# Performance work log

Measured on AMD Instinct MI355X. Metric: run time of the kernel, lower is better.

## Reference

```python
import jax, jax.numpy as jnp
import numpy as np

VOCAB = 32000
EMB = 32
HID = 16
SEQ = 128
BATCH = 32


def setup_inputs() -> dict:
    key = jax.random.key(0)
    k1, k2, k3, k4, k5 = jax.random.split(key, 5)
    return {
        "input_batch": jax.random.randint(k1, (SEQ, BATCH), 0, VOCAB, dtype=jnp.int32),
        "lookup": jax.random.normal(k2, (VOCAB, EMB), dtype=jnp.float32) * 0.1,
        "weight_x": jax.random.normal(k3, (EMB, HID), dtype=jnp.float32) * 0.1,
        "weight_h": jax.random.normal(k4, (HID, HID), dtype=jnp.float32) * 0.1,
        "weight_o": jax.random.normal(k5, (HID, VOCAB), dtype=jnp.float32) * 0.1,
    }


def reference(input_batch, lookup, weight_x, weight_h, weight_o):
    # X: [S, B, EMB]; torch code uses .data -> embedding lookup is detached
    X = jax.lax.stop_gradient(lookup[input_batch])
    batch = input_batch.shape[1]
    H0 = jnp.ones((batch, HID), dtype=jnp.float32)  # torch inits H to ones

    def step(H, x_t):
        H_new = jnp.tanh(x_t @ weight_x + H @ weight_h)  # [B, HID]
        logits = H_new @ weight_o                         # [B, V]
        return H_new, jax.nn.log_softmax(logits, axis=-1)  # log(softmax(x))

    _, out = jax.lax.scan(step, H0, X)  # out: [S, B, V]
    return out
```

## Files before the change

### kernel.cpp

```cpp
#include <hip/hip_runtime.h>

#define VOCAB 32000
#define EMB 32
#define HID 16
#define SEQ 128
#define BATCH 32
#define NROW (SEQ * BATCH)

typedef float f32x2 __attribute__((ext_vector_type(2)));
typedef float f32x4 __attribute__((ext_vector_type(4)));

__global__ __launch_bounds__(512) void embed_xw(
    const int* __restrict__ idx, const float* __restrict__ lookup,
    const float* __restrict__ Wx, float* __restrict__ A)
{
    __shared__ float sWx[EMB][HID];
    const int tid = threadIdx.x;
    ((float*)sWx)[tid] = Wx[tid];
    __syncthreads();

    const int g = blockIdx.x * 512 + tid;
    const int row = g >> 4, j = g & 15;
    const float* xr = lookup + (size_t)idx[row] * EMB;
    float a0 = 0.f, a1 = 0.f;
    #pragma unroll
    for (int e = 0; e < EMB; e += 2) {
        a0 += xr[e] * sWx[e][j];
        a1 += xr[e + 1] * sWx[e + 1][j];
    }
    A[g] = a0 + a1;
}

__global__ __launch_bounds__(512) void rnn_recur(
    const float* __restrict__ A, const float* __restrict__ Wh,
    float* __restrict__ Hout)
{
    __shared__ __align__(16) float sH[BATCH][HID];

    const int tid = threadIdx.x;
    const int b = tid >> 4, j = tid & 15;

    float wh[HID];
    #pragma unroll
    for (int k = 0; k < HID; ++k) wh[k] = Wh[k * HID + j];

    sH[b][j] = 1.0f;
    __syncthreads();

    float a0r = A[0 * 512 + tid];
    float a1r = A[1 * 512 + tid];
    float a2r = A[2 * 512 + tid];
    float a3r = A[3 * 512 + tid];

#define RNN_STEP(AR, T)                                                     \
    {                                                                       \
        float acc = AR;                                                     \
        if ((T) + 4 < SEQ) AR = A[((T) + 4) * 512 + tid];                   \
        const f32x4* sH4 = (const f32x4*)&sH[b][0];                         \
        f32x4 h0 = sH4[0], h1 = sH4[1], h2v = sH4[2], h3v = sH4[3];         \
        acc += h0.x * wh[0] + h0.y * wh[1] + h0.z * wh[2] + h0.w * wh[3];   \
        acc += h1.x * wh[4] + h1.y * wh[5] + h1.z * wh[6] + h1.w * wh[7];   \
        acc += h2v.x * wh[8] + h2v.y * wh[9] + h2v.z * wh[10]               \
             + h2v.w * wh[11];                                              \
        acc += h3v.x * wh[12] + h3v.y * wh[13] + h3v.z * wh[14]             \
             + h3v.w * wh[15];                                              \
        float e2 = __expf(2.f * acc);          \
        float h = 1.f - 2.f / (e2 + 1.f);                                   \
        sH[b][j] = h;                                                       \
        Hout[(T) * 512 + tid] = h;                                          \
    }

    for (int t = 0; t < SEQ; t += 4) {
        RNN_STEP(a0r, t + 0)
        RNN_STEP(a1r, t + 1)
        RNN_STEP(a2r, t + 2)
        RNN_STEP(a3r, t + 3)
    }
#undef RNN_STEP
}

#define CSL 500

__global__ __launch_bounds__(512, 4) void sum_exp_partial(
    const float* __restrict__ H, const float* __restrict__ Wo,
    float* __restrict__ P)
{
    __shared__ float part[8][64];

    const int tid = threadIdx.x;
    const int lane = tid & 63;
    const int wave = tid >> 6;
    const int rgrp = blockIdx.x >> 3;
    const int cchunk = blockIdx.x & 7;
    const int row0 = rgrp * 64;
    const int c0 = __builtin_amdgcn_readfirstlane(cchunk * 4000 + wave * CSL);

    f32x2 hp[HID];
    {
        const f32x4* h4 = (const f32x4*)(H + (size_t)(row0 + lane) * HID);
        #pragma unroll
        for (int q = 0; q < 4; ++q) {
            f32x4 hv = h4[q];
            hp[4 * q + 0] = f32x2{hv.x, hv.x};
            hp[4 * q + 1] = f32x2{hv.y, hv.y};
            hp[4 * q + 2] = f32x2{hv.z, hv.z};
            hp[4 * q + 3] = f32x2{hv.w, hv.w};
        }
    }

    const float* wbase = Wo + c0;
    float acc0 = 0.f, acc1 = 0.f, acc2 = 0.f, acc3 = 0.f;
    for (int v = 0; v < CSL; v += 4) {
        f32x2 a01 = {0.f, 0.f}, a23 = {0.f, 0.f};
        #pragma unroll
        for (int k = 0; k < HID; ++k) {
            f32x4 w4 = *(const f32x4*)(wbase + (size_t)k * VOCAB + v);
            asm("v_pk_fma_f32 %0, %1, %2, %0"
                : "+v"(a01) : "v"(hp[k]), "s"(w4.xy));
            asm("v_pk_fma_f32 %0, %1, %2, %0"
                : "+v"(a23) : "v"(hp[k]), "s"(w4.zw));
        }
        acc0 += __expf(a01.x); acc1 += __expf(a01.y);
        acc2 += __expf(a23.x); acc3 += __expf(a23.y);
    }

    part[wave][lane] = (acc0 + acc1) + (acc2 + acc3);
    __syncthreads();
    if (wave == 0) {
        float tot = 0.f;
        #pragma unroll
        for (int w = 0; w < 8; ++w) tot += part[w][lane];
        P[(size_t)cchunk * NROW + row0 + lane] = tot;
    }
}

#define RV 64
#define VSK 2048

__global__ __launch_bounds__(512, 4) void write_logits(
    const float* __restrict__ H, const float* __restrict__ Wo,
    const float* __restrict__ P, float* __restrict__ out)
{
    __shared__ __align__(16) float sH[RV * HID];
    __shared__ __align__(16) float sLogS[RV];

    const int tid = threadIdx.x;
    const int vtile = blockIdx.x & 15;
    const int row0 = (blockIdx.x >> 4) * RV;

    if (tid < RV * HID / 4)
        *(float4*)(sH + 4 * tid) = *(const float4*)(H + row0 * HID + 4 * tid);
    if (tid < RV) {
        float tot = 0.f;
        #pragma unroll
        for (int p = 0; p < 8; ++p) tot += P[(size_t)p * NROW + row0 + tid];
        sLogS[tid] = __logf(tot);
    }
    __syncthreads();

    const int v = vtile * VSK + 4 * tid;
    if (v >= VOCAB) return;

    f32x2 wlo[HID], whi[HID];
    #pragma unroll
    for (int k = 0; k < HID; ++k) {
        f32x4 w4 = *(const f32x4*)(Wo + (size_t)k * VOCAB + v);
        wlo[k] = w4.xy; whi[k] = w4.zw;
    }
    const f32x4* sH4 = (const f32x4*)sH;
    const f32x4* sLS4 = (const f32x4*)sLogS;

    float* orow = out + (size_t)row0 * VOCAB + v;
    for (int r4 = 0; r4 < RV; r4 += 4) {
        f32x4 ls4 = sLS4[r4 >> 2];
        #pragma unroll
        for (int rr = 0; rr < 4; ++rr) {
            const int r = r4 + rr;
            f32x2 l01 = {0.f, 0.f}, l23 = {0.f, 0.f};
            #pragma unroll
            for (int q = 0; q < 4; ++q) {
                f32x4 hv = sH4[r * 4 + q];
                l01 += hv.x * wlo[4*q+0]; l23 += hv.x * whi[4*q+0];
                l01 += hv.y * wlo[4*q+1]; l23 += hv.y * whi[4*q+1];
                l01 += hv.z * wlo[4*q+2]; l23 += hv.z * whi[4*q+2];
                l01 += hv.w * wlo[4*q+3]; l23 += hv.w * whi[4*q+3];
            }
            const float ls = (rr == 0) ? ls4.x : (rr == 1) ? ls4.y
                           : (rr == 2) ? ls4.z : ls4.w;
            f32x4 o;
            o.xy = l01 - ls;
            o.zw = l23 - ls;
            __builtin_nontemporal_store(o, (f32x4*)orow);
            orow += VOCAB;
        }
    }
}

extern "C" void kernel_launch(void* const* d_in, const int* in_sizes, int n_in,
                              void* d_out, int out_size, void* d_ws, size_t ws_size,
                              hipStream_t stream) {
    const int*   idx    = (const int*)d_in[0];
    const float* lookup = (const float*)d_in[1];
    const float* Wx     = (const float*)d_in[2];
    const float* Wh     = (const float*)d_in[3];
    const float* Wo     = (const float*)d_in[4];
    float* out = (float*)d_out;

    float* Hbuf = (float*)d_ws;
    float* A    = Hbuf + NROW * HID;
    float* P    = A + NROW * HID;

    embed_xw<<<128, 512, 0, stream>>>(idx, lookup, Wx, A);
    rnn_recur<<<1, 512, 0, stream>>>(A, Wh, Hbuf);
    sum_exp_partial<<<512, 512, 0, stream>>>(Hbuf, Wo, P);
    write_logits<<<16 * (NROW / RV), 512, 0, stream>>>(Hbuf, Wo, P, out);
}
```

Baseline: 207.8 us.

## Restructure write_logits to reload Wo per 8-row block and use plain stores

write_logits no longer keeps all 16 Wo columns in registers. For each block of 8 rows it reloads the four Wo vectors per k-group from global memory (likely cache hits) and accumulates 8 rows at once, seeding the accumulator with -logsumexp. The output stores change from nontemporal to normal stores. This cuts register pressure and the per-row subtraction, at the cost of repeated Wo loads and possible cache pollution from the 524MB output stream.

```diff
diff --git a/kernel.cpp b/kernel.cpp
--- a/kernel.cpp
+++ b/kernel.cpp
@@ -136,6 +136,7 @@
 
 #define RV 64
 #define VSK 2048
+#define RB 8
 
 __global__ __launch_bounds__(512, 4) void write_logits(
     const float* __restrict__ H, const float* __restrict__ Wo,
@@ -161,36 +162,35 @@
     const int v = vtile * VSK + 4 * tid;
     if (v >= VOCAB) return;
 
-    f32x2 wlo[HID], whi[HID];
-    #pragma unroll
-    for (int k = 0; k < HID; ++k) {
-        f32x4 w4 = *(const f32x4*)(Wo + (size_t)k * VOCAB + v);
-        wlo[k] = w4.xy; whi[k] = w4.zw;
-    }
+    const float* wp = Wo + v;
     const f32x4* sH4 = (const f32x4*)sH;
-    const f32x4* sLS4 = (const f32x4*)sLogS;
-
-    float* orow = out + (size_t)row0 * VOCAB + v;
-    for (int r4 = 0; r4 < RV; r4 += 4) {
-        f32x4 ls4 = sLS4[r4 >> 2];
-        #pragma unroll
-        for (int rr = 0; rr < 4; ++rr) {
-            const int r = r4 + rr;
-            f32x2 l01 = {0.f, 0.f}, l23 = {0.f, 0.f};
+
+    for (int r8 = 0; r8 < RV; r8 += RB) {
+        f32x4 acc[RB];
+        #pragma unroll
+        for (int r = 0; r < RB; ++r) {
+            float nls = -sLogS[r8 + r];
+            acc[r] = f32x4{nls, nls, nls, nls};
+        }
+        #pragma unroll
+        for (int k4 = 0; k4 < HID / 4; ++k4) {
+            f32x4 w0 = *(const f32x4*)(wp + (size_t)(4 * k4 + 0) * VOCAB);
+            f32x4 w1 = *(const f32x4*)(wp + (size_t)(4 * k4 + 1) * VOCAB);
+            f32x4 w2 = *(const f32x4*)(wp + (size_t)(4 * k4 + 2) * VOCAB);
+            f32x4 w3 = *(const f32x4*)(wp + (size_t)(4 * k4 + 3) * VOCAB);
             #pragma unroll
-            for (int q = 0; q < 4; ++q) {
-                f32x4 hv = sH4[r * 4 + q];
-                l01 += hv.x * wlo[4*q+0]; l23 += hv.x * whi[4*q+0];
-                l01 += hv.y * wlo[4*q+1]; l23 += hv.y * whi[4*q+1];
-                l01 += hv.z * wlo[4*q+2]; l23 += hv.z * whi[4*q+2];
-                l01 += hv.w * wlo[4*q+3]; l23 += hv.w * whi[4*q+3];
+            for (int r = 0; r < RB; ++r) {
+                f32x4 h4 = sH4[(r8 + r) * 4 + k4];
+                acc[r] += h4.x * w0;
+                acc[r] += h4.y * w1;
+                acc[r] += h4.z * w2;
+                acc[r] += h4.w * w3;
             }
-            const float ls = (rr == 0) ? ls4.x : (rr == 1) ? ls4.y
-                           : (rr == 2) ? ls4.z : ls4.w;
-            f32x4 o;
-            o.xy = l01 - ls;
-            o.zw = l23 - ls;
-            __builtin_nontemporal_store(o, (f32x4*)orow);
+        }
+        float* orow = out + (size_t)(row0 + r8) * VOCAB + v;
+        #pragma unroll
+        for (int r = 0; r < RB; ++r) {
+            *(f32x4*)orow = acc[r];
             orow += VOCAB;
         }
     }
```

After: 214.3 us. +3.1%, slower.
